# Kernel tuning notes

Measured on AMD Instinct MI355X. Metric: run time of the kernel, lower is better.

## Reference

```python
import jax, jax.numpy as jnp
import numpy as np

B, T, NODES, D = 8, 32, 400, 64   # batch graphs, time steps, stocks, node_feat_dim==lstm_dim
N = B * T * NODES                 # 102400 total nodes
E = 1_638_400                     # edges (avg degree 16)
L1, L2, FC1, FC2 = 96, 64, 128, 3

def setup_inputs() -> dict:
    key = jax.random.key(0)
    ks = jax.random.split(key, 12)
    rn = lambda k, shape, s=0.05: jax.random.normal(k, shape, jnp.float32) * s
    return {
        "x": jax.random.normal(ks[0], (N, D), jnp.float32),
        "edge_attr": jax.random.normal(ks[1], (E, 2), jnp.float32),
        "conv1_w": rn(ks[2], (D, L1)), "conv1_b": jnp.zeros((L1,), jnp.float32),
        "conv2_w": rn(ks[3], (L1, L2)), "conv2_b": jnp.zeros((L2,), jnp.float32),
        "lstm_w_ih": rn(ks[4], (4 * D, D)), "lstm_w_hh": rn(ks[5], (4 * D, D)),
        "lstm_b_ih": jnp.zeros((4 * D,), jnp.float32), "lstm_b_hh": jnp.zeros((4 * D,), jnp.float32),
        "fc1_w": rn(ks[6], (FC1, L2)), "fc1_b": jnp.zeros((FC1,), jnp.float32),
        "fc2_w": rn(ks[7], (FC2, FC1)), "fc2_b": jnp.zeros((FC2,), jnp.float32),
        "edge_index": jax.random.randint(ks[8], (2, E), 0, N, jnp.int32),
    }

def _normalize(x):
    m = x.mean(axis=0, keepdims=True)
    s = x.std(axis=0, ddof=1, keepdims=True)  # torch.std uses ddof=1
    return (x - m) / s

def _gcn(x, W, b, src, dst, ew):
    """GCNConv with edge weights: add self-loops (weight 1), symmetric norm, scatter-add."""
    n = x.shape[0]
    loops = jnp.arange(n, dtype=src.dtype)
    src2 = jnp.concatenate([src, loops])
    dst2 = jnp.concatenate([dst, loops])
    ew2 = jnp.concatenate([ew, jnp.ones((n,), ew.dtype)])
    deg = jax.ops.segment_sum(ew2, dst2, num_segments=n)
    dis = jnp.where(deg > 0, jax.lax.rsqrt(jnp.where(deg > 0, deg, 1.0)), 0.0)
    norm = dis[src2] * ew2 * dis[dst2]
    h = x @ W                                        # [N, out]
    return jax.ops.segment_sum(h[src2] * norm[:, None], dst2, num_segments=n) + b

def _lstm_last(xseq, w_ih, w_hh, b_ih, b_hh):
    """Single-layer LSTM (torch gate order i,f,g,o); returns last hidden state."""
    Bn = xseq.shape[0]
    H = w_hh.shape[1]
    xg = jnp.einsum('btd,gd->tbg', xseq, w_ih) + (b_ih + b_hh)  # [T, Bn, 4H]
    def step(carry, g_in):
        h, c = carry
        g = g_in + h @ w_hh.T
        i, f, gg, o = jnp.split(g, 4, axis=-1)
        c = jax.nn.sigmoid(f) * c + jax.nn.sigmoid(i) * jnp.tanh(gg)
        h = jax.nn.sigmoid(o) * jnp.tanh(c)
        return (h, c), None
    init = (jnp.zeros((Bn, H), xseq.dtype), jnp.zeros((Bn, H), xseq.dtype))
    (h, _), _ = jax.lax.scan(step, init, xg)
    return h

def reference(x, edge_attr, conv1_w, conv1_b, conv2_w, conv2_b,
              lstm_w_ih, lstm_w_hh, lstm_b_ih, lstm_b_hh,
              fc1_w, fc1_b, fc2_w, fc2_b, edge_index):
    xn = _normalize(x)
    ew = jnp.abs(edge_attr[:, 0])        # args.edgetype = 0
    src, dst = edge_index[0], edge_index[1]
    # (first LSTM over raw x in the original is dead code: output immediately overwritten)
    h = jax.nn.relu(_gcn(xn, conv1_w, conv1_b, src, dst, ew))
    h = jax.nn.relu(_gcn(h, conv2_w, conv2_b, src, dst, ew))
    # to_dense_batch (batch-contiguous nodes) + reshape/permute into per-node time series
    h = h.reshape(B, T, NODES, L2).transpose(0, 2, 1, 3).reshape(B * NODES, T, L2)
    h = _lstm_last(h, lstm_w_ih, lstm_w_hh, lstm_b_ih, lstm_b_hh)   # [B*NODES, L2]
    h = jax.nn.relu(h @ fc1_w.T + fc1_b)
    logits = h @ fc2_w.T + fc2_b
    p = jax.nn.softmax(logits, axis=1)   # softmax over class dim of 2D tensor
    return p.reshape(B, NODES, FC2)
```

## Files before the change

kernel.cpp:

```cpp
#include <hip/hip_runtime.h>
#include <hip/hip_bf16.h>
#include <hip/hip_fp16.h>

#define NN 102400
#define DD 64
#define EE 1638400
#define L1C 96
#define L2C 64
#define TT 32
#define NODESC 400
#define BB 8
#define SS 3200
#define G4 256

#define NBUK 400
#define BCAP 5120
#define PCHUNK 2048
#define NPART (EE / PCHUNK)
#define PTHR 512
#define EPT (PCHUNK / PTHR)

#define OFF_ENT  ((size_t)0)
#define OFF_A1   ((size_t)4096000)
#define OFF_G1   ((size_t)10649600)
#define OFF_ENT2 ((size_t)26214400)
#define OFF_H2   ((size_t)26214400)
#define OFF_G2   ((size_t)32768000)
#define OFF_GCUR ((size_t)39321600)
#define OFF_DIS  ((size_t)39328000)
#define OFF_RNG  ((size_t)39430400)
#define OFF_HL   ((size_t)39635200)
#define OFF_ST   ((size_t)39840000)

typedef __attribute__((ext_vector_type(8))) _Float16 f16x8;
typedef __attribute__((ext_vector_type(4))) float f32x4;

__device__ __forceinline__ void fma4(float4& a, float s, const float4& w) {
    a.x = fmaf(s, w.x, a.x); a.y = fmaf(s, w.y, a.y);
    a.z = fmaf(s, w.z, a.z); a.w = fmaf(s, w.w, a.w);
}
__device__ __forceinline__ float rcp_f(float x) { return __builtin_amdgcn_rcpf(x); }
__device__ __forceinline__ float sigm_f(float x) {
    x = fminf(fmaxf(x, -30.f), 30.f);
    return rcp_f(1.f + __expf(-x));
}
__device__ __forceinline__ float tanh_f(float x) {
    x = fminf(fmaxf(x, -15.f), 15.f);
    float e = __expf(2.f * x);
    return (e - 1.f) * rcp_f(e + 1.f);
}
__device__ __forceinline__ unsigned short f32_bf16_rtne(float f) {
    unsigned int u = __float_as_uint(f);
    unsigned int r = u + 0x7fffu + ((u >> 16) & 1u);
    return (unsigned short)(r >> 16);
}
__device__ __forceinline__ float bf16_f32(unsigned short h) {
    return __uint_as_float(((unsigned int)h) << 16);
}
__device__ __forceinline__ float4 unp4(uint2 p) {
    float4 v;
    v.x = __uint_as_float(p.x << 16);
    v.y = __uint_as_float(p.x & 0xffff0000u);
    v.z = __uint_as_float(p.y << 16);
    v.w = __uint_as_float(p.y & 0xffff0000u);
    return v;
}
__device__ __forceinline__ uint2 pk4(float4 v) {
    unsigned int u0 = ((unsigned int)f32_bf16_rtne(v.y) << 16) | f32_bf16_rtne(v.x);
    unsigned int u1 = ((unsigned int)f32_bf16_rtne(v.w) << 16) | f32_bf16_rtne(v.z);
    return make_uint2(u0, u1);
}
__device__ __forceinline__ uint2 pkh4(float4 v) {
    __half2 h0 = __floats2half2_rn(v.x, v.y);
    __half2 h1 = __floats2half2_rn(v.z, v.w);
    uint2 r;
    r.x = *(unsigned int*)&h0;
    r.y = *(unsigned int*)&h1;
    return r;
}
__device__ __forceinline__ float4 uph4(uint2 p) {
    __half2 h0 = *(__half2*)&p.x;
    __half2 h1 = *(__half2*)&p.y;
    float2 f0 = __half22float2(h0), f1 = __half22float2(h1);
    return make_float4(f0.x, f0.y, f1.x, f1.y);
}

__global__ void init_zero(int* gcur, float* st) {
    int idx = blockIdx.x * 256 + threadIdx.x;
    if (idx < NBUK * 16) gcur[idx] = 0;
    if (blockIdx.x == 0 && threadIdx.x < 128) st[threadIdx.x] = 0.f;
}

__global__ __launch_bounds__(256) void col_sums(const float* __restrict__ x, float* __restrict__ st) {
    int c = threadIdx.x & 63;
    size_t i = (size_t)blockIdx.x * 256 + threadIdx.x;
    size_t stride = (size_t)gridDim.x * 256;
    float s = 0.f, q = 0.f;
    for (size_t e = i; e < (size_t)NN * 64; e += stride) {
        float v = x[e]; s += v; q = fmaf(v, v, q);
    }
    __shared__ float ls[128];
    if (threadIdx.x < 128) ls[threadIdx.x] = 0.f;
    __syncthreads();
    atomicAdd(&ls[c], s); atomicAdd(&ls[64 + c], q);
    __syncthreads();
    if (threadIdx.x < 128) atomicAdd(&st[threadIdx.x], ls[threadIdx.x]);
}

__global__ void finalize_stats(float* st) {
    int c = threadIdx.x;
    if (c < 64) {
        float s = st[c], q = st[64 + c];
        float mean = s / (float)NN;
        float var = (q - s * s / (float)NN) / (float)(NN - 1);
        st[128 + c] = mean;
        st[192 + c] = rsqrtf(fmaxf(var, 1e-20f));
    }
}

__global__ __launch_bounds__(256) void xnd_kernel(const float* __restrict__ x, const float* __restrict__ st,
                                                  const float* __restrict__ dis, uint2* __restrict__ xnd) {
    size_t i = (size_t)blockIdx.x * 256 + threadIdx.x;
    int n = (int)(i >> 4), q = (int)(i & 15);
    float4 v = ((const float4*)x)[i];
    float4 mean4 = ((const float4*)(st + 128))[q];
    float4 istd4 = ((const float4*)(st + 192))[q];
    float dn = dis[n];
    v.x = (v.x - mean4.x) * istd4.x * dn;
    v.y = (v.y - mean4.y) * istd4.y * dn;
    v.z = (v.z - mean4.z) * istd4.z * dn;
    v.w = (v.w - mean4.w) * istd4.w * dn;
    xnd[i] = pk4(v);
}

__global__ __launch_bounds__(PTHR) void part_kernel(const int* __restrict__ ei, const float* __restrict__ ea,
                                                    int* __restrict__ gcur, int2* __restrict__ ent2) {
    __shared__ int lhist[NBUK];
    __shared__ int lbase[NBUK];
    const int tid = threadIdx.x;
    const int e0 = blockIdx.x * PCHUNK;
    for (int i = tid; i < NBUK; i += PTHR) lhist[i] = 0;
    __syncthreads();
    int   dv[EPT]; int sv[EPT]; float wvv[EPT];
    #pragma unroll
    for (int i = 0; i < EPT; ++i) {
        int e = e0 + i * PTHR + tid;
        dv[i]  = ei[EE + e];
        sv[i]  = ei[e];
        wvv[i] = fabsf(ea[2 * (size_t)e]);
        atomicAdd(&lhist[dv[i] >> 8], 1);
    }
    __syncthreads();
    for (int i = tid; i < NBUK; i += PTHR) {
        lbase[i] = atomicAdd(&gcur[i * 16], lhist[i]);
        lhist[i] = 0;
    }
    __syncthreads();
    #pragma unroll
    for (int i = 0; i < EPT; ++i) {
        int d = dv[i];
        int b = d >> 8;
        int local = atomicAdd(&lhist[b], 1);
        int pos = lbase[b] + local;
        if (pos < BCAP)
            ent2[(size_t)b * BCAP + pos] = make_int2(sv[i] | ((d & 255) << 24), __float_as_int(wvv[i]));
    }
}

__global__ __launch_bounds__(256) void bucket_csr(const int2* __restrict__ ent2, const int* __restrict__ gcur,
                                                  int2* __restrict__ ent, int2* __restrict__ rng,
                                                  float* __restrict__ dis) {
    __shared__ int nhist[256];
    __shared__ int scn[256];
    __shared__ float wsum[256];
    __shared__ int pcur[256];
    const int tid = threadIdx.x;
    const int b = blockIdx.x;
    const int base = b * BCAP;
    int cnt = gcur[b * 16];
    if (cnt > BCAP) cnt = BCAP;
    nhist[tid] = 0;
    wsum[tid] = 0.f;
    __syncthreads();
    for (int e = tid; e < cnt; e += 256) {
        int2 en = ent2[base + e];
        int dl = ((unsigned)en.x) >> 24;
        atomicAdd(&nhist[dl], 1);
        atomicAdd(&wsum[dl], __int_as_float(en.y));
    }
    __syncthreads();
    int c = nhist[tid];
    scn[tid] = c;
    __syncthreads();
    for (int d = 1; d < 256; d <<= 1) {
        int t = (tid >= d) ? scn[tid - d] : 0;
        __syncthreads();
        scn[tid] += t;
        __syncthreads();
    }
    int ps = scn[tid] - c;
    rng[b * 256 + tid] = make_int2(base + ps, base + ps + c);
    dis[b * 256 + tid] = rsqrtf(1.f + wsum[tid]);
    pcur[tid] = ps;
    __syncthreads();
    for (int e = tid; e < cnt; e += 256) {
        int2 en = ent2[base + e];
        int dl = ((unsigned)en.x) >> 24;
        int local = atomicAdd(&pcur[dl], 1);
        ent[base + local] = make_int2(en.x & 0xFFFFFF, en.y);
    }
}

template<int K, int NC, int MB, int THREADS, bool PRELU, bool DISO, bool HIN, bool HOUT>
__global__ __launch_bounds__(THREADS) void gemm_tiled(
    const float* __restrict__ A, const float* __restrict__ Wm,
    const float* __restrict__ bin, const float* __restrict__ dscale,
    float* __restrict__ Cm, int ldC)
{
    __shared__ float As[MB * K];
    __shared__ float Ws[K * NC];

    for (int i = threadIdx.x; i < K * NC / 4; i += THREADS)
        ((float4*)Ws)[i] = ((const float4*)Wm)[i];

    size_t row0 = (size_t)blockIdx.x * MB;
    for (int i = threadIdx.x; i < MB * (K / 4); i += THREADS) {
        int r = i / (K / 4); int c = (i % (K / 4)) * 4;
        float4 a;
        if (HIN) {
            uint2 p = *(const uint2*)((const unsigned short*)A + (row0 + r) * K + c);
            a = uph4(p);
        } else {
            a = *(const float4*)(A + (row0 + r) * K + c);
        }
        if (PRELU) {
            a.x = fmaxf(a.x + bin[c + 0], 0.f); a.y = fmaxf(a.y + bin[c + 1], 0.f);
            a.z = fmaxf(a.z + bin[c + 2], 0.f); a.w = fmaxf(a.w + bin[c + 3], 0.f);
        }
        ((float4*)As)[i] = a;
    }
    __syncthreads();

    constexpr int NCT = NC / 4;
    int tc = threadIdx.x % NCT;
    int tr = threadIdx.x / NCT;
    int r = tr * 4;
    float4 acc[4];
    acc[0] = acc[1] = acc[2] = acc[3] = make_float4(0.f, 0.f, 0.f, 0.f);

    #pragma unroll 8
    for (int d4 = 0; d4 < K / 4; ++d4) {
        float4 w0 = ((const float4*)Ws)[(4 * d4 + 0) * NCT + tc];
        float4 w1 = ((const float4*)Ws)[(4 * d4 + 1) * NCT + tc];
        float4 w2 = ((const float4*)Ws)[(4 * d4 + 2) * NCT + tc];
        float4 w3 = ((const float4*)Ws)[(4 * d4 + 3) * NCT + tc];
        #pragma unroll
        for (int i = 0; i < 4; ++i) {
            float4 av = ((const float4*)As)[(r + i) * (K / 4) + d4];
            fma4(acc[i], av.x, w0); fma4(acc[i], av.y, w1);
            fma4(acc[i], av.z, w2); fma4(acc[i], av.w, w3);
        }
    }

    #pragma unroll
    for (int i = 0; i < 4; ++i) {
        size_t row = row0 + r + i;
        float4 o = acc[i];
        if (DISO) {
            float dn = dscale[row];
            o.x *= dn; o.y *= dn; o.z *= dn; o.w *= dn;
            *(uint2*)((unsigned short*)Cm + row * ldC + tc * 4) = pk4(o);
        } else if (HOUT) {
            *(uint2*)((unsigned short*)Cm + row * ldC + tc * 4) = pkh4(o);
        } else {
            *(float4*)(Cm + row * ldC + tc * 4) = o;
        }
    }
}

template<int C4>
__global__ __launch_bounds__(256) void gcn_gather(const uint2* __restrict__ h, const int2* __restrict__ rng,
                                                  const int2* __restrict__ ent, const float* __restrict__ dis,
                                                  unsigned short* __restrict__ g) {
    unsigned int idx = blockIdx.x * 256 + threadIdx.x;
    unsigned int n = idx / C4, q = idx % C4;
    float4 acc = unp4(h[(size_t)n * C4 + q]);
    int2 r = rng[n];
    int e = r.x;
    for (; e + 8 <= r.y; e += 8) {
        int2 en0 = ent[e],     en1 = ent[e + 1], en2 = ent[e + 2], en3 = ent[e + 3];
        int2 en4 = ent[e + 4], en5 = ent[e + 5], en6 = ent[e + 6], en7 = ent[e + 7];
        uint2 v0 = h[(size_t)en0.x * C4 + q];
        uint2 v1 = h[(size_t)en1.x * C4 + q];
        uint2 v2 = h[(size_t)en2.x * C4 + q];
        uint2 v3 = h[(size_t)en3.x * C4 + q];
        uint2 v4 = h[(size_t)en4.x * C4 + q];
        uint2 v5 = h[(size_t)en5.x * C4 + q];
        uint2 v6 = h[(size_t)en6.x * C4 + q];
        uint2 v7 = h[(size_t)en7.x * C4 + q];
        fma4(acc, __int_as_float(en0.y), unp4(v0));
        fma4(acc, __int_as_float(en1.y), unp4(v1));
        fma4(acc, __int_as_float(en2.y), unp4(v2));
        fma4(acc, __int_as_float(en3.y), unp4(v3));
        fma4(acc, __int_as_float(en4.y), unp4(v4));
        fma4(acc, __int_as_float(en5.y), unp4(v5));
        fma4(acc, __int_as_float(en6.y), unp4(v6));
        fma4(acc, __int_as_float(en7.y), unp4(v7));
    }
    for (; e + 4 <= r.y; e += 4) {
        int2 en0 = ent[e], en1 = ent[e + 1], en2 = ent[e + 2], en3 = ent[e + 3];
        uint2 v0 = h[(size_t)en0.x * C4 + q];
        uint2 v1 = h[(size_t)en1.x * C4 + q];
        uint2 v2 = h[(size_t)en2.x * C4 + q];
        uint2 v3 = h[(size_t)en3.x * C4 + q];
        fma4(acc, __int_as_float(en0.y), unp4(v0));
        fma4(acc, __int_as_float(en1.y), unp4(v1));
        fma4(acc, __int_as_float(en2.y), unp4(v2));
        fma4(acc, __int_as_float(en3.y), unp4(v3));
    }
    for (; e < r.y; ++e) {
        int2 en = ent[e];
        uint2 v = h[(size_t)en.x * C4 + q];
        fma4(acc, __int_as_float(en.y), unp4(v));
    }
    float dn = dis[n];
    acc.x *= dn; acc.y *= dn; acc.z *= dn; acc.w *= dn;
    *(uint2*)(g + (size_t)n * (C4 * 4) + q * 4) = pkh4(acc);
}

#define XP_LD 72
#define HP_LD2 72
#define GP_LD 258

__global__ __launch_bounds__(1024, 1) void lstm_kernel(
    const __half* __restrict__ g2, const float* __restrict__ cb2,
    const float* __restrict__ whh, const float* __restrict__ wih,
    const float* __restrict__ bih, const float* __restrict__ bhh,
    float* __restrict__ hlast)
{
    __shared__ __align__(16) _Float16 xpack[32 * 16 * XP_LD];
    __shared__ __align__(16) _Float16 hhi[16 * HP_LD2];
    __shared__ __align__(16) _Float16 hlo[16 * HP_LD2];
    __shared__ float gp[16 * GP_LD];
    const int tid  = threadIdx.x;
    const int lane = tid & 63;
    const int wv   = tid >> 6;
    const int n15  = lane & 15;
    const int quad = lane >> 4;
    const int gate = wv * 16 + n15;
    const int qa   = wv;
    const int ja   = lane;

    f16x8 whh_h[2], whh_l[2], wih_h[2], wih_l[2];
    {
        const float* wp = whh + (size_t)gate * 64 + quad * 8;
        const float* xp = wih + (size_t)gate * 64 + quad * 8;
        #pragma unroll
        for (int kc = 0; kc < 2; ++kc) {
            #pragma unroll
            for (int j = 0; j < 8; ++j) {
                float w = wp[kc * 32 + j];
                _Float16 h = (_Float16)w;
                whh_h[kc][j] = h;
                whh_l[kc][j] = (_Float16)((w - (float)h) * 2048.f);
                float v = xp[kc * 32 + j];
                _Float16 g = (_Float16)v;
                wih_h[kc][j] = g;
                wih_l[kc][j] = (_Float16)((v - (float)g) * 2048.f);
            }
        }
    }

    const float bi_i = bih[ja]        + bhh[ja];
    const float bi_f = bih[64 + ja]   + bhh[64 + ja];
    const float bi_g = bih[128 + ja]  + bhh[128 + ja];
    const float bi_o = bih[192 + ja]  + bhh[192 + ja];

    {
        const int s0 = blockIdx.x * 16;
        const int b_ = s0 / NODESC;
        const int node0 = s0 - b_ * NODESC;
        const int r  = (tid >> 4) & 15;
        const int c4 = tid & 15;
        const int t0 = tid >> 8;
        float4 bias4 = *(const float4*)(cb2 + c4 * 4);
        _Float16* dst = xpack + r * XP_LD + c4 * 4;
        const __half* src = g2 + ((size_t)(b_ * TT + t0) * NODESC + node0 + r) * 64 + c4 * 4;
        #pragma unroll
        for (int i = 0; i < 8; ++i) {
            uint2 p = *(const uint2*)(src + (size_t)i * 4 * NODESC * 64);
            float4 v = uph4(p);
            v.x = fmaxf(v.x + bias4.x, 0.f);
            v.y = fmaxf(v.y + bias4.y, 0.f);
            v.z = fmaxf(v.z + bias4.z, 0.f);
            v.w = fmaxf(v.w + bias4.w, 0.f);
            *(uint2*)(dst + (size_t)(t0 + i * 4) * (16 * XP_LD)) = pkh4(v);
        }
    }

    for (int i = tid; i < 16 * HP_LD2; i += 1024) { hhi[i] = (_Float16)0.f; hlo[i] = (_Float16)0.f; }
    float c_reg = 0.f, hn = 0.f;
    __syncthreads();

    const int xbase = n15 * XP_LD + quad * 8;
    const int hbase = n15 * HP_LD2 + quad * 8;

    for (int t = 0; t < TT; ++t) {
        f32x4 cm  = {0.f, 0.f, 0.f, 0.f};
        f32x4 cl0 = {0.f, 0.f, 0.f, 0.f};
        f32x4 cl1 = {0.f, 0.f, 0.f, 0.f};
        const _Float16* xrow = xpack + (size_t)t * (16 * XP_LD);
        {
            f16x8 ax0 = *(const f16x8*)(xrow + xbase);
            f16x8 ah0 = *(const f16x8*)(hhi + hbase);
            f16x8 al0 = *(const f16x8*)(hlo + hbase);
            f16x8 ax1 = *(const f16x8*)(xrow + xbase + 32);
            f16x8 ah1 = *(const f16x8*)(hhi + hbase + 32);
            f16x8 al1 = *(const f16x8*)(hlo + hbase + 32);
            cm  = __builtin_amdgcn_mfma_f32_16x16x32_f16(ax0, wih_h[0], cm,  0, 0, 0);
            cl0 = __builtin_amdgcn_mfma_f32_16x16x32_f16(ax0, wih_l[0], cl0, 0, 0, 0);
            cl1 = __builtin_amdgcn_mfma_f32_16x16x32_f16(ax1, wih_l[1], cl1, 0, 0, 0);
            cm  = __builtin_amdgcn_mfma_f32_16x16x32_f16(ah0, whh_h[0], cm,  0, 0, 0);
            cl0 = __builtin_amdgcn_mfma_f32_16x16x32_f16(al0, whh_h[0], cl0, 0, 0, 0);
            cl1 = __builtin_amdgcn_mfma_f32_16x16x32_f16(al1, whh_h[1], cl1, 0, 0, 0);
            cm  = __builtin_amdgcn_mfma_f32_16x16x32_f16(ax1, wih_h[1], cm,  0, 0, 0);
            cl0 = __builtin_amdgcn_mfma_f32_16x16x32_f16(ah0, whh_l[0], cl0, 0, 0, 0);
            cl1 = __builtin_amdgcn_mfma_f32_16x16x32_f16(ah1, whh_l[1], cl1, 0, 0, 0);
            cm  = __builtin_amdgcn_mfma_f32_16x16x32_f16(ah1, whh_h[1], cm,  0, 0, 0);
        }
        f32x4 c = cm + (cl0 + cl1) * (1.f / 2048.f);
        #pragma unroll
        for (int r = 0; r < 4; ++r)
            gp[(quad * 4 + r) * GP_LD + gate] = c[r];
        __syncthreads();

        {
            float gi = gp[qa * GP_LD + ja]        + bi_i;
            float gf = gp[qa * GP_LD + 64 + ja]   + bi_f;
            float gg = gp[qa * GP_LD + 128 + ja]  + bi_g;
            float go = gp[qa * GP_LD + 192 + ja]  + bi_o;
            c_reg = sigm_f(gf) * c_reg + sigm_f(gi) * tanh_f(gg);
            hn = sigm_f(go) * tanh_f(c_reg);
            _Float16 hh = (_Float16)hn;
            hhi[qa * HP_LD2 + ja] = hh;
            hlo[qa * HP_LD2 + ja] = (_Float16)((hn - (float)hh) * 2048.f);
        }
        __syncthreads();
    }
    hlast[((size_t)blockIdx.x * 16 + qa) * 64 + ja] = hn;
}

__global__ __launch_bounds__(128) void head_kernel(const float* __restrict__ hl,
                                                   const float* __restrict__ w1, const float* __restrict__ b1,
                                                   const float* __restrict__ w2, const float* __restrict__ b2,
                                                   float* __restrict__ out) {
    __shared__ float hrow[64];
    __shared__ float a1[128];
    __shared__ float lg[3];
    int s = blockIdx.x, tid = threadIdx.x;
    if (tid < 64) hrow[tid] = hl[(size_t)s * 64 + tid];
    __syncthreads();
    {
        const float4* wr = (const float4*)(w1 + (size_t)tid * 64);
        const float4* hq = (const float4*)hrow;
        float4 acc = make_float4(0.f, 0.f, 0.f, 0.f);
        #pragma unroll
        for (int k = 0; k < 16; ++k) {
            float4 wv = wr[k]; float4 hv = hq[k];
            acc.x = fmaf(wv.x, hv.x, acc.x); acc.y = fmaf(wv.y, hv.y, acc.y);
            acc.z = fmaf(wv.z, hv.z, acc.z); acc.w = fmaf(wv.w, hv.w, acc.w);
        }
        a1[tid] = fmaxf((acc.x + acc.y) + (acc.z + acc.w) + b1[tid], 0.f);
    }
    __syncthreads();
    if (tid < 3) {
        const float4* wr = (const float4*)(w2 + (size_t)tid * 128);
        const float4* aq = (const float4*)a1;
        float4 acc = make_float4(0.f, 0.f, 0.f, 0.f);
        #pragma unroll
        for (int k = 0; k < 32; ++k) {
            float4 wv = wr[k]; float4 av = aq[k];
            acc.x = fmaf(wv.x, av.x, acc.x); acc.y = fmaf(wv.y, av.y, acc.y);
            acc.z = fmaf(wv.z, av.z, acc.z); acc.w = fmaf(wv.w, av.w, acc.w);
        }
        lg[tid] = (acc.x + acc.y) + (acc.z + acc.w) + b2[tid];
    }
    __syncthreads();
    if (tid == 0) {
        float m = fmaxf(lg[0], fmaxf(lg[1], lg[2]));
        float e0 = __expf(lg[0] - m), e1 = __expf(lg[1] - m), e2 = __expf(lg[2] - m);
        float inv = 1.f / (e0 + e1 + e2);
        out[(size_t)s * 3 + 0] = e0 * inv;
        out[(size_t)s * 3 + 1] = e1 * inv;
        out[(size_t)s * 3 + 2] = e2 * inv;
    }
}

extern "C" void kernel_launch(void* const* d_in, const int* in_sizes, int n_in,
                              void* d_out, int out_size, void* d_ws, size_t ws_size,
                              hipStream_t stream) {
    (void)in_sizes; (void)n_in; (void)out_size; (void)ws_size;
    const float* x        = (const float*)d_in[0];
    const float* ea       = (const float*)d_in[1];
    const float* conv1_w  = (const float*)d_in[2];
    const float* conv1_b  = (const float*)d_in[3];
    const float* conv2_w  = (const float*)d_in[4];
    const float* conv2_b  = (const float*)d_in[5];
    const float* w_ih     = (const float*)d_in[6];
    const float* w_hh     = (const float*)d_in[7];
    const float* b_ih     = (const float*)d_in[8];
    const float* b_hh     = (const float*)d_in[9];
    const float* fc1_w    = (const float*)d_in[10];
    const float* fc1_b    = (const float*)d_in[11];
    const float* fc2_w    = (const float*)d_in[12];
    const float* fc2_b    = (const float*)d_in[13];
    const int*   ei       = (const int*)d_in[14];
    float* out = (float*)d_out;

    float* W    = (float*)d_ws;
    int2*  ent  = (int2*)(W + OFF_ENT);
    unsigned short* a1h = (unsigned short*)(W + OFF_A1);
    unsigned short* g1h = (unsigned short*)(W + OFF_G1);
    int2*  ent2 = (int2*)(W + OFF_ENT2);
    uint2* xnd  = (uint2*)(W + OFF_ENT2);
    float* h2   = W + OFF_H2;
    unsigned short* g2h = (unsigned short*)(W + OFF_G2);
    int*   gcur = (int*)(W + OFF_GCUR);
    float* dis  = W + OFF_DIS;
    int2*  rng  = (int2*)(W + OFF_RNG);
    float* hl   = W + OFF_HL;
    float* st   = W + OFF_ST;

    init_zero<<<26, 256, 0, stream>>>(gcur, st);
    col_sums<<<1024, 256, 0, stream>>>(x, st);
    finalize_stats<<<1, 64, 0, stream>>>(st);

    part_kernel<<<NPART, PTHR, 0, stream>>>(ei, ea, gcur, ent2);
    bucket_csr<<<NBUK, 256, 0, stream>>>(ent2, gcur, ent, rng, dis);

    xnd_kernel<<<NN * 16 / 256, 256, 0, stream>>>(x, st, dis, xnd);

    gcn_gather<16><<<NN * 16 / 256, 256, 0, stream>>>(xnd, rng, ent, dis, a1h);
    gemm_tiled<64, 96, 32, 192, false, false, true, true><<<NN / 32, 192, 0, stream>>>(
        (const float*)a1h, conv1_w, nullptr, nullptr, (float*)g1h, 96);

    gemm_tiled<96, 64, 64, 256, true, true, true, false><<<NN / 64, 256, 0, stream>>>(
        (const float*)g1h, conv2_w, conv1_b, dis, h2, 64);
    gcn_gather<16><<<NN * 16 / 256, 256, 0, stream>>>((const uint2*)h2, rng, ent, dis, g2h);

    lstm_kernel<<<SS / 16, 1024, 0, stream>>>((const __half*)g2h, conv2_b, w_hh, w_ih,
                                              b_ih, b_hh, hl);

    head_kernel<<<SS, 128, 0, stream>>>(hl, fc1_w, fc1_b, fc2_w, fc2_b, out);
}
```

Baseline: 385.6 us.

## Restructure LSTM kernel so each wave owns all four gates, removing gate LDS exchange

The LSTM block shrinks from 1024 to 256 threads. Each wave now computes all four gate tiles for its 16 hidden units, so the cell update happens directly on the MFMA accumulators instead of going through a shared gate buffer. The hidden state is double-buffered in LDS, which cuts the per-step barriers from two to one and removes the gate scatter/gather through shared memory. The cost is four times the weight registers per thread and four times the MFMAs per wave, with fewer waves in flight per block, which could lower latency hiding or occupancy.

```diff
diff --git a/kernel.cpp b/kernel.cpp
--- a/kernel.cpp
+++ b/kernel.cpp
@@ -330,124 +330,143 @@
 
 #define XP_LD 72
 #define HP_LD2 72
-#define GP_LD 258
-
-__global__ __launch_bounds__(1024, 1) void lstm_kernel(
+
+__global__ __launch_bounds__(256, 1) void lstm_kernel(
     const __half* __restrict__ g2, const float* __restrict__ cb2,
     const float* __restrict__ whh, const float* __restrict__ wih,
     const float* __restrict__ bih, const float* __restrict__ bhh,
     float* __restrict__ hlast)
 {
     __shared__ __align__(16) _Float16 xpack[32 * 16 * XP_LD];
-    __shared__ __align__(16) _Float16 hhi[16 * HP_LD2];
-    __shared__ __align__(16) _Float16 hlo[16 * HP_LD2];
-    __shared__ float gp[16 * GP_LD];
+    __shared__ __align__(16) _Float16 hhi[2][16 * HP_LD2];
+    __shared__ __align__(16) _Float16 hlo[2][16 * HP_LD2];
     const int tid  = threadIdx.x;
     const int lane = tid & 63;
     const int wv   = tid >> 6;
     const int n15  = lane & 15;
     const int quad = lane >> 4;
-    const int gate = wv * 16 + n15;
-    const int qa   = wv;
-    const int ja   = lane;
-
-    f16x8 whh_h[2], whh_l[2], wih_h[2], wih_l[2];
-    {
+    const int j    = wv * 16 + n15;
+
+    f16x8 whhh[4][2], whhl[4][2], wihh[4][2], wihl[4][2];
+    #pragma unroll
+    for (int gt = 0; gt < 4; ++gt) {
+        const int gate = gt * 64 + j;
         const float* wp = whh + (size_t)gate * 64 + quad * 8;
         const float* xp = wih + (size_t)gate * 64 + quad * 8;
         #pragma unroll
         for (int kc = 0; kc < 2; ++kc) {
             #pragma unroll
-            for (int j = 0; j < 8; ++j) {
-                float w = wp[kc * 32 + j];
+            for (int jj = 0; jj < 8; ++jj) {
+                float w = wp[kc * 32 + jj];
                 _Float16 h = (_Float16)w;
-                whh_h[kc][j] = h;
-                whh_l[kc][j] = (_Float16)((w - (float)h) * 2048.f);
-                float v = xp[kc * 32 + j];
+                whhh[gt][kc][jj] = h;
+                whhl[gt][kc][jj] = (_Float16)((w - (float)h) * 2048.f);
+                float v = xp[kc * 32 + jj];
                 _Float16 g = (_Float16)v;
-                wih_h[kc][j] = g;
-                wih_l[kc][j] = (_Float16)((v - (float)g) * 2048.f);
+                wihh[gt][kc][jj] = g;
+                wihl[gt][kc][jj] = (_Float16)((v - (float)g) * 2048.f);
             }
         }
     }
 
-    const float bi_i = bih[ja]        + bhh[ja];
-    const float bi_f = bih[64 + ja]   + bhh[64 + ja];
-    const float bi_g = bih[128 + ja]  + bhh[128 + ja];
-    const float bi_o = bih[192 + ja]  + bhh[192 + ja];
+    const float bi0 = bih[j]        + bhh[j];
+    const float bi1 = bih[64 + j]   + bhh[64 + j];
+    const float bi2 = bih[128 + j]  + bhh[128 + j];
+    const float bi3 = bih[192 + j]  + bhh[192 + j];
 
     {
         const int s0 = blockIdx.x * 16;
         const int b_ = s0 / NODESC;
         const int node0 = s0 - b_ * NODESC;
-        const int r  = (tid >> 4) & 15;
+        const int r  = tid >> 4;
         const int c4 = tid & 15;
-        const int t0 = tid >> 8;
         float4 bias4 = *(const float4*)(cb2 + c4 * 4);
         _Float16* dst = xpack + r * XP_LD + c4 * 4;
-        const __half* src = g2 + ((size_t)(b_ * TT + t0) * NODESC + node0 + r) * 64 + c4 * 4;
-        #pragma unroll
-        for (int i = 0; i < 8; ++i) {
-            uint2 p = *(const uint2*)(src + (size_t)i * 4 * NODESC * 64);
+        const __half* src = g2 + ((size_t)(b_ * TT) * NODESC + node0 + r) * 64 + c4 * 4;
+        #pragma unroll 8
+        for (int t = 0; t < TT; ++t) {
+            uint2 p = *(const uint2*)(src + (size_t)t * NODESC * 64);
             float4 v = uph4(p);
             v.x = fmaxf(v.x + bias4.x, 0.f);
             v.y = fmaxf(v.y + bias4.y, 0.f);
             v.z = fmaxf(v.z + bias4.z, 0.f);
             v.w = fmaxf(v.w + bias4.w, 0.f);
-            *(uint2*)(dst + (size_t)(t0 + i * 4) * (16 * XP_LD)) = pkh4(v);
-        }
-    }
-
-    for (int i = tid; i < 16 * HP_LD2; i += 1024) { hhi[i] = (_Float16)0.f; hlo[i] = (_Float16)0.f; }
-    float c_reg = 0.f, hn = 0.f;
-    __syncthreads();
-
-    const int xbase = n15 * XP_LD + quad * 8;
-    const int hbase = n15 * HP_LD2 + quad * 8;
+            *(uint2*)(dst + (size_t)t * (16 * XP_LD)) = pkh4(v);
+        }
+    }
+
+    for (int i = tid; i < 16 * HP_LD2; i += 256) {
+        hhi[0][i] = (_Float16)0.f; hlo[0][i] = (_Float16)0.f;
+    }
+    float creg[4] = {0.f, 0.f, 0.f, 0.f};
+    float hreg[4] = {0.f, 0.f, 0.f, 0.f};
+    __syncthreads();
+
+    const int xb = n15 * XP_LD + quad * 8;
+    const int hb = n15 * HP_LD2 + quad * 8;
 
     for (int t = 0; t < TT; ++t) {
-        f32x4 cm  = {0.f, 0.f, 0.f, 0.f};
-        f32x4 cl0 = {0.f, 0.f, 0.f, 0.f};
-        f32x4 cl1 = {0.f, 0.f, 0.f, 0.f};
+        const int cur = t & 1;
+        const int nxt = cur ^ 1;
+        f32x4 cm[4], cl0[4], cl1[4];
+        #pragma unroll
+        for (int gt = 0; gt < 4; ++gt) {
+            cm[gt]  = (f32x4){0.f, 0.f, 0.f, 0.f};
+            cl0[gt] = (f32x4){0.f, 0.f, 0.f, 0.f};
+            cl1[gt] = (f32x4){0.f, 0.f, 0.f, 0.f};
+        }
         const _Float16* xrow = xpack + (size_t)t * (16 * XP_LD);
-        {
-            f16x8 ax0 = *(const f16x8*)(xrow + xbase);
-            f16x8 ah0 = *(const f16x8*)(hhi + hbase);
-            f16x8 al0 = *(const f16x8*)(hlo + hbase);
-            f16x8 ax1 = *(const f16x8*)(xrow + xbase + 32);
-            f16x8 ah1 = *(const f16x8*)(hhi + hbase + 32);
-            f16x8 al1 = *(const f16x8*)(hlo + hbase + 32);
-            cm  = __builtin_amdgcn_mfma_f32_16x16x32_f16(ax0, wih_h[0], cm,  0, 0, 0);
-            cl0 = __builtin_amdgcn_mfma_f32_16x16x32_f16(ax0, wih_l[0], cl0, 0, 0, 0);
-            cl1 = __builtin_amdgcn_mfma_f32_16x16x32_f16(ax1, wih_l[1], cl1, 0, 0, 0);
-            cm  = __builtin_amdgcn_mfma_f32_16x16x32_f16(ah0, whh_h[0], cm,  0, 0, 0);
-            cl0 = __builtin_amdgcn_mfma_f32_16x16x32_f16(al0, whh_h[0], cl0, 0, 0, 0);
-            cl1 = __builtin_amdgcn_mfma_f32_16x16x32_f16(al1, whh_h[1], cl1, 0, 0, 0);
-            cm  = __builtin_amdgcn_mfma_f32_16x16x32_f16(ax1, wih_h[1], cm,  0, 0, 0);
-            cl0 = __builtin_amdgcn_mfma_f32_16x16x32_f16(ah0, whh_l[0], cl0, 0, 0, 0);
-            cl1 = __builtin_amdgcn_mfma_f32_16x16x32_f16(ah1, whh_l[1], cl1, 0, 0, 0);
-            cm  = __builtin_amdgcn_mfma_f32_16x16x32_f16(ah1, whh_h[1], cm,  0, 0, 0);
-        }
-        f32x4 c = cm + (cl0 + cl1) * (1.f / 2048.f);
-        #pragma unroll
-        for (int r = 0; r < 4; ++r)
-            gp[(quad * 4 + r) * GP_LD + gate] = c[r];
+        f16x8 ax0 = *(const f16x8*)(xrow + xb);
+        f16x8 ax1 = *(const f16x8*)(xrow + xb + 32);
+        f16x8 ah0 = *(const f16x8*)(&hhi[cur][hb]);
+        f16x8 ah1 = *(const f16x8*)(&hhi[cur][hb + 32]);
+        f16x8 al0 = *(const f16x8*)(&hlo[cur][hb]);
+        f16x8 al1 = *(const f16x8*)(&hlo[cur][hb + 32]);
+        #pragma unroll
+        for (int gt = 0; gt < 4; ++gt) {
+            cm[gt]  = __builtin_amdgcn_mfma_f32_16x16x32_f16(ax0, wihh[gt][0], cm[gt],  0, 0, 0);
+            cl0[gt] = __builtin_amdgcn_mfma_f32_16x16x32_f16(ax0, wihl[gt][0], cl0[gt], 0, 0, 0);
+        }
+        #pragma unroll
+        for (int gt = 0; gt < 4; ++gt) {
+            cm[gt]  = __builtin_amdgcn_mfma_f32_16x16x32_f16(ah0, whhh[gt][0], cm[gt],  0, 0, 0);
+            cl0[gt] = __builtin_amdgcn_mfma_f32_16x16x32_f16(al0, whhh[gt][0], cl0[gt], 0, 0, 0);
+            cl1[gt] = __builtin_amdgcn_mfma_f32_16x16x32_f16(ax1, wihl[gt][1], cl1[gt], 0, 0, 0);
+        }
+        #pragma unroll
+        for (int gt = 0; gt < 4; ++gt) {
+            cm[gt]  = __builtin_amdgcn_mfma_f32_16x16x32_f16(ax1, wihh[gt][1], cm[gt],  0, 0, 0);
+            cl0[gt] = __builtin_amdgcn_mfma_f32_16x16x32_f16(ah0, whhl[gt][0], cl0[gt], 0, 0, 0);
+            cl1[gt] = __builtin_amdgcn_mfma_f32_16x16x32_f16(al1, whhh[gt][1], cl1[gt], 0, 0, 0);
+        }
+        #pragma unroll
+        for (int gt = 0; gt < 4; ++gt) {
+            cm[gt]  = __builtin_amdgcn_mfma_f32_16x16x32_f16(ah1, whhh[gt][1], cm[gt],  0, 0, 0);
+            cl1[gt] = __builtin_amdgcn_mfma_f32_16x16x32_f16(ah1, whhl[gt][1], cl1[gt], 0, 0, 0);
+        }
+        f32x4 g0 = cm[0] + (cl0[0] + cl1[0]) * (1.f / 2048.f);
+        f32x4 g1 = cm[1] + (cl0[1] + cl1[1]) * (1.f / 2048.f);
+        f32x4 g2v = cm[2] + (cl0[2] + cl1[2]) * (1.f / 2048.f);
+        f32x4 g3 = cm[3] + (cl0[3] + cl1[3]) * (1.f / 2048.f);
+
+        #pragma unroll
+        for (int r = 0; r < 4; ++r) {
+            float gi = g0[r] + bi0;
+            float gf = g1[r] + bi1;
+            float gg = g2v[r] + bi2;
+            float go = g3[r] + bi3;
+            creg[r] = sigm_f(gf) * creg[r] + sigm_f(gi) * tanh_f(gg);
+            hreg[r] = sigm_f(go) * tanh_f(creg[r]);
+            _Float16 hh = (_Float16)hreg[r];
+            const int row = quad * 4 + r;
+            hhi[nxt][row * HP_LD2 + j] = hh;
+            hlo[nxt][row * HP_LD2 + j] = (_Float16)((hreg[r] - (float)hh) * 2048.f);
+        }
         __syncthreads();
-
-        {
-            float gi = gp[qa * GP_LD + ja]        + bi_i;
-            float gf = gp[qa * GP_LD + 64 + ja]   + bi_f;
-            float gg = gp[qa * GP_LD + 128 + ja]  + bi_g;
-            float go = gp[qa * GP_LD + 192 + ja]  + bi_o;
-            c_reg = sigm_f(gf) * c_reg + sigm_f(gi) * tanh_f(gg);
-            hn = sigm_f(go) * tanh_f(c_reg);
-            _Float16 hh = (_Float16)hn;
-            hhi[qa * HP_LD2 + ja] = hh;
-            hlo[qa * HP_LD2 + ja] = (_Float16)((hn - (float)hh) * 2048.f);
-        }
-        __syncthreads();
-    }
-    hlast[((size_t)blockIdx.x * 16 + qa) * 64 + ja] = hn;
+    }
+    #pragma unroll
+    for (int r = 0; r < 4; ++r)
+        hlast[((size_t)blockIdx.x * 16 + quad * 4 + r) * 64 + j] = hreg[r];
 }
 
 __global__ __launch_bounds__(128) void head_kernel(const float* __restrict__ hl,
@@ -548,8 +567,8 @@
         (const float*)g1h, conv2_w, conv1_b, dis, h2, 64);
     gcn_gather<16><<<NN * 16 / 256, 256, 0, stream>>>((const uint2*)h2, rng, ent, dis, g2h);
 
-    lstm_kernel<<<SS / 16, 1024, 0, stream>>>((const __half*)g2h, conv2_b, w_hh, w_ih,
-                                              b_ih, b_hh, hl);
+    lstm_kernel<<<SS / 16, 256, 0, stream>>>((const __half*)g2h, conv2_b, w_hh, w_ih,
+                                             b_ih, b_hh, hl);
 
     head_kernel<<<SS, 128, 0, stream>>>(hl, fc1_w, fc1_b, fc2_w, fc2_b, out);
 }
```

After: 385.8 us. No clear change (+0.1%).
